# Kernel optimization log

Hardware: AMD Instinct MI355X
Metric: run time of the kernel (lower is better)

The kernel has to match this reference:

```python
import jax, jax.numpy as jnp
import numpy as np

B, NUM_ANCHORS, NUM_CLASSES = 32, 15130, 81
SCALE_XY, SCALE_WH = 0.1, 0.2
CRITERIA, MAX_OUT, SCORE_THRESH = 0.5, 200, 0.05


def setup_inputs() -> dict:
    key = jax.random.key(0)
    k1, k2, k3, k4 = jax.random.split(key, 4)
    ploc = jax.random.normal(k1, (B, 4, NUM_ANCHORS), dtype=jnp.float32)
    plabel = jax.random.normal(k2, (B, NUM_CLASSES, NUM_ANCHORS), dtype=jnp.float32)
    # default boxes in (cx, cy, w, h) form, all in [0, 1]
    xy = jax.random.uniform(k3, (NUM_ANCHORS, 2), dtype=jnp.float32, minval=0.05, maxval=0.95)
    wh = jax.random.uniform(k4, (NUM_ANCHORS, 2), dtype=jnp.float32, minval=0.02, maxval=0.3)
    dboxes_xywh = jnp.concatenate([xy, wh], axis=-1)
    return {"ploc": ploc, "plabel": plabel, "dboxes_xywh": dboxes_xywh}


def _iou(a, b):
    # a: [M,4] ltrb, b: [K,4] ltrb -> [M,K]
    lt = jnp.maximum(a[:, None, :2], b[None, :, :2])
    rb = jnp.minimum(a[:, None, 2:], b[None, :, 2:])
    wh = jnp.clip(rb - lt, 0.0)
    inter = wh[..., 0] * wh[..., 1]
    area_a = (a[:, 2] - a[:, 0]) * (a[:, 3] - a[:, 1])
    area_b = (b[:, 2] - b[:, 0]) * (b[:, 3] - b[:, 1])
    return inter / (area_a[:, None] + area_b[None, :] - inter + 1e-12)


def _decode(ploc, plabel, dboxes_xywh):
    # scale_back_batch: ploc [B,4,N] -> ltrb boxes [B,N,4]
    b = jnp.transpose(ploc, (0, 2, 1))
    xy = b[..., :2] * SCALE_XY * dboxes_xywh[:, 2:] + dboxes_xywh[:, :2]
    wh = jnp.exp(b[..., 2:] * SCALE_WH) * dboxes_xywh[:, 2:]
    ltrb = jnp.concatenate([xy - 0.5 * wh, xy + 0.5 * wh], axis=-1)  # [B,N,4]
    probs = jnp.transpose(jax.nn.softmax(plabel, axis=1), (0, 2, 1))  # [B,N,C]
    return ltrb, probs


def _nms_per_class(scores_c, boxes):
    # scores_c: [N], boxes: [N,4]
    s = jnp.where(scores_c > SCORE_THRESH, scores_c, 0.0)
    vals, idx = jax.lax.top_k(s, MAX_OUT)  # descending, matches score-sorted greedy order
    bx = boxes[idx]  # [MAX_OUT,4]
    iou = _iou(bx, bx)  # [MAX_OUT,MAX_OUT]
    later = jnp.arange(MAX_OUT)

    def body(i, keep):
        active = keep[i] & (vals[i] > 0.0)
        suppress = active & (iou[i] >= CRITERIA) & (later > i)
        return keep & ~suppress

    keep = jax.lax.fori_loop(0, MAX_OUT, body, jnp.ones((MAX_OUT,), bool))
    keep = keep & (vals > 0.0)
    return jnp.where(keep, vals, 0.0), bx


def _decode_single(probs_i, boxes_i):
    # skip background class 0
    cls_scores = probs_i[:, 1:].T  # [C-1, N]
    vals, bx = jax.vmap(_nms_per_class, in_axes=(0, None))(cls_scores, boxes_i)
    c1 = NUM_CLASSES - 1
    flat_v = vals.reshape(-1)                 # [(C-1)*MAX_OUT]
    flat_b = bx.reshape(-1, 4)
    labels = jnp.repeat(jnp.arange(1, c1 + 1, dtype=jnp.int32), MAX_OUT)
    top_v, top_i = jax.lax.top_k(flat_v, MAX_OUT)
    return flat_b[top_i], labels[top_i], top_v


def reference(ploc, plabel, dboxes_xywh):
    ltrb, probs = _decode(ploc, plabel, dboxes_xywh)
    boxes_out, labels_out, scores_out = jax.vmap(_decode_single)(probs, ltrb)
    return boxes_out, labels_out, scores_out
```

## Files before the change

kernel.cpp:

```cpp
#include <hip/hip_runtime.h>
#include <math.h>

namespace {
constexpr int BATCH = 32;
constexpr int NANCH = 15130;
constexpr int NCLS  = 81;
constexpr int C1    = 80;
constexpr int MAXO  = 200;
constexpr int APB   = 256;
constexpr int NBLKA = (NANCH + APB - 1) / APB;
constexpr int CAPK2 = 512;
constexpr int CAP   = 1024;
constexpr int CAPB  = 768;
constexpr int NWORD = 4;
constexpr int NBIN  = 2048;
constexpr int NBINK2 = 768;
constexpr unsigned BINBASE = 0x3D000000u;
constexpr int IMGCAP = C1 * MAXO;
}

#define SCORE_TH 0.05f
#define IOU_TH   0.5f

typedef unsigned long long u64;

__device__ __forceinline__ u64 shflx64(u64 v, int mask) {
    int lo = __shfl_xor((int)(unsigned)(v & 0xffffffffull), mask, 64);
    int hi = __shfl_xor((int)(unsigned)(v >> 32), mask, 64);
    return ((u64)(unsigned)hi << 32) | (unsigned)lo;
}

__device__ __forceinline__ void bitonic_desc(u64* keys, int P,
                                             int tid, int nthr) {
    for (int k = 2; k <= P; k <<= 1) {
        for (int j = k >> 1; j > 0; j >>= 1) {
            for (int i = tid; i < P; i += nthr) {
                int ixj = i ^ j;
                if (ixj > i) {
                    u64 a = keys[i], c = keys[ixj];
                    bool up = ((i & k) == 0);
                    if (up ? (a < c) : (a > c)) { keys[i] = c; keys[ixj] = a; }
                }
            }
            __syncthreads();
        }
    }
}

__device__ __forceinline__ u64 regsort256(u64 key, u64* lds, int tid) {
    for (int k = 2; k <= 256; k <<= 1) {
        for (int j = k >> 1; j > 0; j >>= 1) {
            u64 pv;
            if (j < 64) {
                pv = shflx64(key, j);
            } else {
                lds[tid] = key;
                __syncthreads();
                pv = lds[tid ^ j];
            }
            bool up = ((tid & k) == 0);
            bool lt = ((tid & j) == 0);
            u64 mx = (key > pv) ? key : pv;
            u64 mn = (key > pv) ? pv : key;
            key = (up == lt) ? mx : mn;
            if (j >= 64) __syncthreads();
        }
    }
    return key;
}

__global__ __launch_bounds__(256, 3) void ssd_decode_stats(
    const float* __restrict__ ploc, const float* __restrict__ plabel,
    const float* __restrict__ dboxes,
    float* __restrict__ ltrb, float* __restrict__ rowmax,
    float* __restrict__ rowsum,
    int* __restrict__ cntg, u64* __restrict__ bucket) {
#pragma clang fp contract(off)
    __shared__ int lcnt[C1], lbase[C1], lrank[C1];

    const int tid = threadIdx.x;
    const int b   = blockIdx.x / NBLKA;
    const int n0  = (blockIdx.x % NBLKA) * APB;
    const int n   = n0 + tid;
    const bool act = (n < NANCH);

    if (tid < C1) lcnt[tid] = 0;

    float x[NCLS];
    if (act) {
        const float* pl = ploc + (size_t)b * 4 * NANCH + n;
        float px = pl[0], py = pl[NANCH], pw = pl[2 * NANCH],
              ph = pl[3 * NANCH];
        float4 db = reinterpret_cast<const float4*>(dboxes)[n];
        float cx = px * 0.1f * db.z + db.x;
        float cy = py * 0.1f * db.w + db.y;
        float w  = expf(pw * 0.2f) * db.z;
        float h  = expf(ph * 0.2f) * db.w;
        float4 o;
        o.x = cx - 0.5f * w; o.y = cy - 0.5f * h;
        o.z = cx + 0.5f * w; o.w = cy + 0.5f * h;
        reinterpret_cast<float4*>(ltrb)[(size_t)b * NANCH + n] = o;

        const float* pb = plabel + (size_t)b * NCLS * NANCH + n;
#pragma unroll
        for (int c = 0; c < NCLS; ++c) x[c] = pb[(size_t)c * NANCH];

        float m = -INFINITY;
#pragma unroll
        for (int c = 0; c < NCLS; ++c) m = fmaxf(m, x[c]);
#pragma unroll
        for (int c = 0; c < NCLS; ++c) x[c] = expf(x[c] - m);
        float s = 0.f;
#pragma unroll
        for (int c = 0; c < NCLS; ++c) s += x[c];
        rowmax[(size_t)b * NANCH + n] = m;
        rowsum[(size_t)b * NANCH + n] = s;

#pragma unroll
        for (int c = 1; c < NCLS; ++c) {
            x[c] = x[c] / s;
            if (x[c] > SCORE_TH) atomicAdd(&lcnt[c - 1], 1);
        }
    }
    __syncthreads();

    if (tid < C1) {
        int cn = lcnt[tid];
        lbase[tid] = (cn > 0) ? atomicAdd(&cntg[b * C1 + tid], cn) : 0;
        lrank[tid] = 0;
    }
    __syncthreads();

    if (act) {
#pragma unroll
        for (int c = 1; c < NCLS; ++c) {
            if (x[c] > SCORE_TH) {
                int r = atomicAdd(&lrank[c - 1], 1);
                int pos = lbase[c - 1] + r;
                if (pos < CAPB)
                    bucket[(size_t)(b * C1 + (c - 1)) * CAPB + pos] =
                        ((u64)__float_as_uint(x[c]) << 32)
                        | (u64)(0xFFFFFFFFu - (unsigned)n);
            }
        }
    }
}

__global__ __launch_bounds__(256, 8) void ssd_class_nms(
    const float* __restrict__ plabel, const float* __restrict__ rowmax,
    const float* __restrict__ rowsum, const float* __restrict__ ltrb,
    const int* __restrict__ cntg, const u64* __restrict__ bucket,
    float* __restrict__ pcVals, float* __restrict__ pcBoxes,
    int* __restrict__ imgcnt, u64* __restrict__ imglist) {
    __shared__ u64 cand[CAPK2];
    __shared__ unsigned int hist[NBINK2];
    __shared__ float4 box4[MAXO];
    __shared__ float areas[MAXO], vs[MAXO];
    __shared__ u64 supflat[MAXO * NWORD];
    __shared__ u64 keepw[NWORD], vmaskS[NWORD];
    __shared__ int wtot[4];
    __shared__ int cnt, fillcnt, cutbin, kcnt, kbase;

    const int tid  = threadIdx.x;
    const int lane = tid & 63;
    const int wv   = tid >> 6;
    const int b    = blockIdx.x / C1;
    const int cls  = blockIdx.x % C1 + 1;
    const int bc   = b * C1 + (cls - 1);

    for (int i = tid; i < NBINK2; i += 256) hist[i] = 0u;
    if (tid == 0) { cnt = 0; fillcnt = 0; cutbin = 1; kcnt = 0; }
    __syncthreads();

    const float* pl = plabel + ((size_t)b * NCLS + cls) * NANCH;
    const float* rm = rowmax + (size_t)b * NANCH;
    const float* rs = rowsum + (size_t)b * NANCH;
    const u64* bkt = bucket + (size_t)bc * CAPB;

    const int gcount = cntg[bc];
    const bool ovf = (gcount > CAPB);
    int gathered;

    if (!ovf) {
        const int count = gcount;
        for (int i = tid; i < count; i += 256) {
            unsigned bits = (unsigned)(bkt[i] >> 32);
            unsigned bin = ((bits - BINBASE) >> 16) + 1u;
            if (bin > NBINK2 - 1) bin = NBINK2 - 1;
            atomicAdd(&hist[bin], 1u);
        }
        __syncthreads();

        const int base = tid * 3;
        int loc = (int)hist[base] + (int)hist[base + 1] + (int)hist[base + 2];
        int sfx = loc;
        for (int off = 1; off < 64; off <<= 1) {
            int t = __shfl_down(sfx, off, 64);
            if (lane + off < 64) sfx += t;
        }
        if (lane == 0) wtot[wv] = sfx;
        __syncthreads();
        int crossSuf = 0;
        for (int w2 = wv + 1; w2 < 4; ++w2) crossSuf += wtot[w2];
        const int nztot = wtot[0] + wtot[1] + wtot[2] + wtot[3];
        {
            int S = (sfx - loc) + crossSuf;
            for (int k = 2; k >= 0; --k) {
                int binv = (int)hist[base + k];
                int Sk = S + binv;
                int bin = base + k;
                if (bin >= 1 && Sk >= MAXO && S < MAXO) cutbin = bin;
                S = Sk;
            }
        }
        __syncthreads();
        const int B = (nztot >= MAXO) ? cutbin : 1;

        for (int i = tid; i < count; i += 256) {
            u64 k = bkt[i];
            unsigned bits = (unsigned)(k >> 32);
            unsigned bin = ((bits - BINBASE) >> 16) + 1u;
            if (bin > NBINK2 - 1) bin = NBINK2 - 1;
            if ((int)bin >= B) {
                int pos = atomicAdd(&cnt, 1);
                if (pos < CAPK2) cand[pos] = k;
            }
        }
        __syncthreads();
        gathered = min(cnt, CAPK2);
    } else {
        for (int n = tid; n < NANCH; n += 256) {
            float p = expf(pl[n] - rm[n]) / rs[n];
            if (p > SCORE_TH) {
                int pos = atomicAdd(&cnt, 1);
                if (pos < CAPK2)
                    cand[pos] = ((u64)__float_as_uint(p) << 32)
                              | (u64)(0xFFFFFFFFu - (unsigned)n);
            }
        }
        __syncthreads();
        gathered = min(cnt, CAPK2);
    }

    u64 key;
    if (gathered <= 256) {
        key = (tid < gathered) ? cand[tid] : 0ull;
        key = regsort256(key, cand, tid);
    } else {
        for (int i = gathered + tid; i < CAPK2; i += 256) cand[i] = 0ull;
        __syncthreads();
        bitonic_desc(cand, CAPK2, tid, 256);
        key = cand[tid];
    }

    if (gathered < MAXO) {
        int* scanb = (int*)hist;
        cand[tid] = key;
        __syncthreads();
        const int need = MAXO - gathered;
        for (int base2 = 0; base2 < NANCH; base2 += 256) {
            if (fillcnt >= need) break;
            int n = base2 + tid;
            int flag = 0;
            if (n < NANCH) {
                float p = expf(pl[n] - rm[n]) / rs[n];
                flag = (p <= SCORE_TH) ? 1 : 0;
            }
            scanb[tid] = flag;
            __syncthreads();
            for (int off = 1; off < 256; off <<= 1) {
                int v  = scanb[tid];
                int vp = (tid >= off) ? scanb[tid - off] : 0;
                __syncthreads();
                scanb[tid] = v + vp;
                __syncthreads();
            }
            int excl = scanb[tid] - flag;
            if (flag && (fillcnt + excl) < need)
                cand[gathered + fillcnt + excl] =
                    (u64)(0xFFFFFFFFu - (unsigned)n);
            __syncthreads();
            if (tid == 0) fillcnt += scanb[255];
            __syncthreads();
        }
        __syncthreads();
        key = cand[tid];
    }

    if (tid < MAXO) {
#pragma clang fp contract(off)
        float sc   = __uint_as_float((unsigned)(key >> 32));
        unsigned n = 0xFFFFFFFFu - (unsigned)(key & 0xFFFFFFFFull);
        float4 bb =
            reinterpret_cast<const float4*>(ltrb)[(size_t)b * NANCH + n];
        box4[tid] = bb;
        areas[tid] = (bb.z - bb.x) * (bb.w - bb.y);
        vs[tid] = sc;
    }
    {
        bool pred = (tid < MAXO) ?
            (__uint_as_float((unsigned)(key >> 32)) > 0.f) : false;
        u64 bal = __ballot(pred);
        if (lane == 0) vmaskS[wv] = bal;
    }
    __syncthreads();

    if (tid < MAXO) {
#pragma clang fp contract(off)
        const int i = tid;
        float4 bi = box4[i];
        float ai = areas[i];
        for (int w = 0; w < NWORD; ++w) {
            int j0 = max(i + 1, w * 64);
            int j1 = min(MAXO, w * 64 + 64);
            u64 m = 0ull;
            for (int j = j0; j < j1; ++j) {
                float4 bj = box4[j];
                float l = fmaxf(bi.x, bj.x);
                float t = fmaxf(bi.y, bj.y);
                float r = fminf(bi.z, bj.z);
                float d = fminf(bi.w, bj.w);
                float ww = fmaxf(r - l, 0.f);
                float hh = fmaxf(d - t, 0.f);
                float inter = ww * hh;
                float denom = ai + areas[j] - inter + 1e-12f;
                float t2 = inter + inter;
                bool sup_t = (t2 >= denom);
                bool band = (t2 < denom) && (t2 > denom * 0.99999952f);
                if (__any(band))
                    sup_t = band ? ((inter / denom) >= IOU_TH) : sup_t;
                m |= sup_t ? (1ull << (j - w * 64)) : 0ull;
            }
            supflat[i * NWORD + w] = m;
        }
    }
    __syncthreads();

    if (tid == 0) {
        u64 v0 = vmaskS[0], v1 = vmaskS[1], v2 = vmaskS[2], v3 = vmaskS[3];
        u64 k0 = ~0ull, k1 = ~0ull, k2 = ~0ull, k3 = ~0ull;
        for (int w = 0; w < 4; ++w) {
            u64 vw = (w == 0) ? v0 : (w == 1) ? v1 : (w == 2) ? v2 : v3;
            u64 kw = (w == 0) ? k0 : (w == 1) ? k1 : (w == 2) ? k2 : k3;
            u64 cur = kw & vw;
            while (cur) {
                int bit = __builtin_ctzll(cur);
                int i = w * 64 + bit;
                k0 &= ~supflat[i * NWORD + 0];
                k1 &= ~supflat[i * NWORD + 1];
                k2 &= ~supflat[i * NWORD + 2];
                k3 &= ~supflat[i * NWORD + 3];
                kw = (w == 0) ? k0 : (w == 1) ? k1 : (w == 2) ? k2 : k3;
                u64 above = (bit == 63) ? 0ull : (~0ull << (bit + 1));
                cur = kw & vw & above;
            }
        }
        keepw[0] = k0; keepw[1] = k1; keepw[2] = k2; keepw[3] = k3;
    }
    __syncthreads();

    bool kp = false;
    if (tid < MAXO) {
        kp = (keepw[tid >> 6] >> (tid & 63)) & 1ull;
        pcVals[(size_t)bc * MAXO + tid] = (kp && vs[tid] > 0.f) ? vs[tid] : 0.f;
        reinterpret_cast<float4*>(pcBoxes + (size_t)bc * MAXO * 4)[tid] =
            box4[tid];
    }

    bool keep_me = (tid < MAXO) && kp && (vs[tid] > 0.f);
    int r = -1;
    if (keep_me) r = atomicAdd(&kcnt, 1);
    __syncthreads();
    if (tid == 0) kbase = (kcnt > 0) ? atomicAdd(&imgcnt[b], kcnt) : 0;
    __syncthreads();
    if (keep_me) {
        unsigned g = (unsigned)((cls - 1) * MAXO + tid);
        imglist[(size_t)b * IMGCAP + kbase + r] =
            ((u64)__float_as_uint(vs[tid]) << 32) | (u64)(0xFFFFFFFFu - g);
    }
}

__global__ __launch_bounds__(256) void ssd_final_topk(
    const float* __restrict__ pcVals, const float* __restrict__ pcBoxes,
    const int* __restrict__ imgcnt, const u64* __restrict__ imglist,
    float* __restrict__ out) {
    __shared__ unsigned int hist[NBIN];
    __shared__ u64 cand[CAP];
    __shared__ int wtot[4];
    __shared__ int cnt, cutbin, nztot;

    const int tid  = threadIdx.x;
    const int lane = tid & 63;
    const int wv   = tid >> 6;
    const int b    = blockIdx.x;
    const int TOT  = C1 * MAXO;
    const float* pv = pcVals + (size_t)b * TOT;
    const int NZ   = imgcnt[b];

    for (int i = tid; i < NBIN; i += 256) hist[i] = 0u;
    if (tid == 0) { cnt = 0; cutbin = 1; }
    __syncthreads();

    int count;
    if (NZ >= MAXO) {
        const u64* lst = imglist + (size_t)b * IMGCAP;
        for (int i = tid; i < NZ; i += 256) {
            unsigned bits = (unsigned)(lst[i] >> 32);
            unsigned bin = ((bits - BINBASE) >> 15) + 1u;
            if (bin > NBIN - 1) bin = NBIN - 1;
            atomicAdd(&hist[bin], 1u);
        }
        __syncthreads();

        const int base = tid * 8;
        int loc = 0;
        for (int k = 0; k < 8; ++k) loc += (int)hist[base + k];
        int sfx = loc;
        for (int off = 1; off < 64; off <<= 1) {
            int t = __shfl_down(sfx, off, 64);
            if (lane + off < 64) sfx += t;
        }
        if (lane == 0) wtot[wv] = sfx;
        __syncthreads();
        int crossSuf = 0;
        for (int w2 = wv + 1; w2 < 4; ++w2) crossSuf += wtot[w2];
        {
            int S = (sfx - loc) + crossSuf;
            for (int k = 7; k >= 0; --k) {
                int binv = (int)hist[base + k];
                int Sk = S + binv;
                int bin = base + k;
                if (bin >= 1 && Sk >= MAXO && S < MAXO) cutbin = bin;
                S = Sk;
            }
        }
        __syncthreads();
        const int B = cutbin;

        for (int i = tid; i < NZ; i += 256) {
            u64 k = lst[i];
            unsigned bits = (unsigned)(k >> 32);
            unsigned bin = ((bits - BINBASE) >> 15) + 1u;
            if (bin > NBIN - 1) bin = NBIN - 1;
            if ((int)bin >= B) {
                int pos = atomicAdd(&cnt, 1);
                if (pos < CAP) cand[pos] = k;
            }
        }
        __syncthreads();
        count = min(cnt, CAP);
    } else {
        for (int g = tid; g < TOT; g += 256) {
            float v = pv[g];
            if (v > 0.f) {
                unsigned bits = __float_as_uint(v);
                unsigned bin = ((bits - BINBASE) >> 15) + 1u;
                if (bin > NBIN - 1) bin = NBIN - 1;
                atomicAdd(&hist[bin], 1u);
            }
        }
        __syncthreads();
        const int base = tid * 8;
        int loc = 0;
        for (int k = 0; k < 8; ++k) loc += (int)hist[base + k];
        int sfx = loc;
        for (int off = 1; off < 64; off <<= 1) {
            int t = __shfl_down(sfx, off, 64);
            if (lane + off < 64) sfx += t;
        }
        if (lane == 0) wtot[wv] = sfx;
        __syncthreads();
        int crossSuf = 0;
        for (int w2 = wv + 1; w2 < 4; ++w2) crossSuf += wtot[w2];
        if (tid == 0) nztot = wtot[0] + wtot[1] + wtot[2] + wtot[3];
        {
            int S = (sfx - loc) + crossSuf;
            for (int k = 7; k >= 0; --k) {
                int binv = (int)hist[base + k];
                int Sk = S + binv;
                int bin = base + k;
                if (bin >= 1 && Sk >= MAXO && S < MAXO) cutbin = bin;
                S = Sk;
            }
        }
        __syncthreads();
        int B = (nztot >= MAXO) ? cutbin : 1;

        for (int g = tid; g < TOT; g += 256) {
            float v = pv[g];
            if (v > 0.f) {
                unsigned bits = __float_as_uint(v);
                unsigned bin = ((bits - BINBASE) >> 15) + 1u;
                if (bin > NBIN - 1) bin = NBIN - 1;
                if ((int)bin >= B) {
                    int pos = atomicAdd(&cnt, 1);
                    if (pos < CAP)
                        cand[pos] = ((u64)bits << 32)
                                  | (u64)(0xFFFFFFFFu - (unsigned)g);
                }
            }
        }
        __syncthreads();
        count = min(cnt, CAP);

        if (count < MAXO) {
            if (tid == 0) {
                int c = count;
                for (int g = 0; g < TOT && c < MAXO; ++g) {
                    if (!(pv[g] > 0.f)) {
                        cand[c++] = (u64)(0xFFFFFFFFu - (unsigned)g);
                    }
                }
                cnt = c;
            }
            __syncthreads();
            count = min(cnt, CAP);
        }
    }

    u64 key;
    if (count <= 256) {
        key = (tid < count) ? cand[tid] : 0ull;
        key = regsort256(key, cand, tid);
    } else {
        int P = 256; while (P < count) P <<= 1;
        for (int i = count + tid; i < P; i += 256) cand[i] = 0ull;
        __syncthreads();
        bitonic_desc(cand, P, tid, 256);
        key = cand[tid];
    }

    if (tid < MAXO) {
        float sc      = __uint_as_float((unsigned)(key >> 32));
        unsigned flat = 0xFFFFFFFFu - (unsigned)(key & 0xFFFFFFFFull);
        int cls = (int)(flat / MAXO) + 1;
        const float4 bb =
            reinterpret_cast<const float4*>(pcBoxes)[(size_t)b * TOT + flat];
        reinterpret_cast<float4*>(out)[(size_t)b * MAXO + tid] = bb;
        out[(size_t)BATCH * MAXO * 4 + (size_t)b * MAXO + tid] = (float)cls;
        out[(size_t)BATCH * MAXO * 5 + (size_t)b * MAXO + tid] = sc;
    }
}

extern "C" void kernel_launch(void* const* d_in, const int* in_sizes, int n_in,
                              void* d_out, int out_size, void* d_ws,
                              size_t ws_size, hipStream_t stream) {
    const float* ploc   = (const float*)d_in[0];
    const float* plabel = (const float*)d_in[1];
    const float* dboxes = (const float*)d_in[2];
    float* out = (float*)d_out;

    float* ws      = (float*)d_ws;
    float* ltrb    = ws;
    float* rowmax  = ltrb   + (size_t)BATCH * NANCH * 4;
    float* rowsum  = rowmax + (size_t)BATCH * NANCH;
    float* pcVals  = rowsum + (size_t)BATCH * NANCH;
    float* pcBoxes = pcVals + (size_t)BATCH * C1 * MAXO;
    int*   cntg    = (int*)(pcBoxes + (size_t)BATCH * C1 * MAXO * 4);
    int*   imgcnt  = cntg + BATCH * C1;
    char*  after   = (char*)(imgcnt + BATCH);
    u64* bucket = (u64*)(after + ((16 - (((size_t)after) & 15)) & 15));
    u64* imglist = bucket + (size_t)BATCH * C1 * CAPB;

    hipMemsetAsync(cntg, 0, (size_t)(BATCH * C1 + BATCH) * sizeof(int), stream);
    ssd_decode_stats<<<BATCH * NBLKA, APB, 0, stream>>>(
        ploc, plabel, dboxes, ltrb, rowmax, rowsum, cntg, bucket);
    ssd_class_nms<<<BATCH * C1, 256, 0, stream>>>(
        plabel, rowmax, rowsum, ltrb, cntg, bucket, pcVals, pcBoxes,
        imgcnt, imglist);
    ssd_final_topk<<<BATCH, 256, 0, stream>>>(
        pcVals, pcBoxes, imgcnt, imglist, out);
}
```

Baseline: 238.6 us.

## Parallelize IoU suppression mask build across lanes using ballots per row

Rebuilds the pairwise IoU suppression bitmask so that each lane handles one column j and each wave iterates over rows i, producing each 64-bit word with a wave ballot. Before, one thread per row walked a serial j loop. Only the triangular region is computed, and the greedy scan skips reading words it can never need. This spreads the O(MAXO^2) IoU work across all four wavefronts and removes divergent per-thread loops. In exchange it adds ballot overhead and a serial i loop per wave.

```diff
diff --git a/kernel.cpp b/kernel.cpp
--- a/kernel.cpp
+++ b/kernel.cpp
@@ -305,17 +305,18 @@
     }
     __syncthreads();
 
-    if (tid < MAXO) {
+    {
 #pragma clang fp contract(off)
-        const int i = tid;
-        float4 bi = box4[i];
-        float ai = areas[i];
-        for (int w = 0; w < NWORD; ++w) {
-            int j0 = max(i + 1, w * 64);
-            int j1 = min(MAXO, w * 64 + 64);
-            u64 m = 0ull;
-            for (int j = j0; j < j1; ++j) {
-                float4 bj = box4[j];
+#pragma unroll
+        for (int c = 0; c < NWORD; ++c) {
+            const int jc = c * 64 + lane;
+            const bool jv = (jc < MAXO);
+            const float4 bj = box4[jv ? jc : 0];
+            const float aj = areas[jv ? jc : 0];
+            const int iend = (MAXO < c * 64 + 64) ? MAXO : (c * 64 + 64);
+            for (int i = wv; i < iend; i += 4) {
+                float4 bi = box4[i];
+                float ai = areas[i];
                 float l = fmaxf(bi.x, bj.x);
                 float t = fmaxf(bi.y, bj.y);
                 float r = fminf(bi.z, bj.z);
@@ -323,15 +324,24 @@
                 float ww = fmaxf(r - l, 0.f);
                 float hh = fmaxf(d - t, 0.f);
                 float inter = ww * hh;
-                float denom = ai + areas[j] - inter + 1e-12f;
+                float denom = ai + aj - inter + 1e-12f;
                 float t2 = inter + inter;
-                bool sup_t = (t2 >= denom);
-                bool band = (t2 < denom) && (t2 > denom * 0.99999952f);
-                if (__any(band))
-                    sup_t = band ? ((inter / denom) >= IOU_TH) : sup_t;
-                m |= sup_t ? (1ull << (j - w * 64)) : 0ull;
-            }
-            supflat[i * NWORD + w] = m;
+                u64 supb  = __ballot(t2 >= denom);
+                u64 bandb = __ballot((t2 < denom) &&
+                                     (t2 > denom * 0.99999952f));
+                u64 valid = (c == 3) ? ((1ull << (MAXO - 192)) - 1ull) : ~0ull;
+                if (i >= c * 64) {
+                    int sh = i - c * 64 + 1;
+                    valid &= (sh >= 64) ? 0ull : (~0ull << sh);
+                }
+                supb &= valid;
+                bandb &= valid & ~supb;
+                if (bandb) {
+                    u64 divb = __ballot(jv && ((inter / denom) >= IOU_TH));
+                    supb = (supb & ~bandb) | (divb & bandb);
+                }
+                if (lane == 0) supflat[i * NWORD + c] = supb;
+            }
         }
     }
     __syncthreads();
@@ -346,9 +356,9 @@
             while (cur) {
                 int bit = __builtin_ctzll(cur);
                 int i = w * 64 + bit;
-                k0 &= ~supflat[i * NWORD + 0];
-                k1 &= ~supflat[i * NWORD + 1];
-                k2 &= ~supflat[i * NWORD + 2];
+                if (w == 0) k0 &= ~supflat[i * NWORD + 0];
+                if (w <= 1) k1 &= ~supflat[i * NWORD + 1];
+                if (w <= 2) k2 &= ~supflat[i * NWORD + 2];
                 k3 &= ~supflat[i * NWORD + 3];
                 kw = (w == 0) ? k0 : (w == 1) ? k1 : (w == 2) ? k2 : k3;
                 u64 above = (bit == 63) ? 0ull : (~0ull << (bit + 1));
```

New measurement: 241.2 us. Within noise of the previous version (+1.1%).

## Replace full IoU bitmask NMS with iterative keep-driven suppression rounds

Applied to the files above, without the earlier changes.

Drops the precomputed 200x200 suppression bitmask and the serial single-thread scan. NMS now runs greedily: each round picks the next kept candidate, every thread tests its own box against it, and a ballot clears suppressed bits. This does IoU work only for kept boxes and frees shared memory, which may raise occupancy. The cost is two block barriers per kept box, which can be many when few boxes overlap, and an exact division per test.

```diff
diff --git a/kernel.cpp b/kernel.cpp
--- a/kernel.cpp
+++ b/kernel.cpp
@@ -156,10 +156,9 @@
     __shared__ unsigned int hist[NBINK2];
     __shared__ float4 box4[MAXO];
     __shared__ float areas[MAXO], vs[MAXO];
-    __shared__ u64 supflat[MAXO * NWORD];
-    __shared__ u64 keepw[NWORD], vmaskS[NWORD];
+    __shared__ u64 keepw[NWORD], vmaskS[NWORD], supRow[NWORD];
     __shared__ int wtot[4];
-    __shared__ int cnt, fillcnt, cutbin, kcnt, kbase;
+    __shared__ int cnt, fillcnt, cutbin, kcnt, kbase, curI;
 
     const int tid  = threadIdx.x;
     const int lane = tid & 63;
@@ -287,87 +286,96 @@
         key = cand[tid];
     }
 
+    float4 bjr = make_float4(0.f, 0.f, 0.f, 0.f);
+    float ajr = 0.f, vsr = 0.f;
     if (tid < MAXO) {
 #pragma clang fp contract(off)
-        float sc   = __uint_as_float((unsigned)(key >> 32));
+        vsr = __uint_as_float((unsigned)(key >> 32));
         unsigned n = 0xFFFFFFFFu - (unsigned)(key & 0xFFFFFFFFull);
-        float4 bb =
-            reinterpret_cast<const float4*>(ltrb)[(size_t)b * NANCH + n];
-        box4[tid] = bb;
-        areas[tid] = (bb.z - bb.x) * (bb.w - bb.y);
-        vs[tid] = sc;
+        bjr = reinterpret_cast<const float4*>(ltrb)[(size_t)b * NANCH + n];
+        ajr = (bjr.z - bjr.x) * (bjr.w - bjr.y);
+        box4[tid] = bjr;
+        areas[tid] = ajr;
+        vs[tid] = vsr;
     }
     {
-        bool pred = (tid < MAXO) ?
-            (__uint_as_float((unsigned)(key >> 32)) > 0.f) : false;
+        bool pred = (tid < MAXO) && (vsr > 0.f);
         u64 bal = __ballot(pred);
         if (lane == 0) vmaskS[wv] = bal;
     }
-    __syncthreads();
-
-    if (tid < MAXO) {
+    if (tid == 0) {
+        keepw[0] = ~0ull; keepw[1] = ~0ull; keepw[2] = ~0ull; keepw[3] = ~0ull;
+    }
+    __syncthreads();
+
+    if (tid == 0) {
+        int ni = -1;
+        u64 c0 = keepw[0] & vmaskS[0];
+        if (c0) ni = __builtin_ctzll(c0);
+        else {
+            u64 c1 = keepw[1] & vmaskS[1];
+            if (c1) ni = 64 + __builtin_ctzll(c1);
+            else {
+                u64 c2 = keepw[2] & vmaskS[2];
+                if (c2) ni = 128 + __builtin_ctzll(c2);
+                else {
+                    u64 c3 = keepw[3] & vmaskS[3];
+                    if (c3) ni = 192 + __builtin_ctzll(c3);
+                }
+            }
+        }
+        curI = ni;
+    }
+    __syncthreads();
+
+    while (true) {
+        const int i = curI;
+        if (i < 0) break;
+        bool sup = false;
+        if (tid > i && tid < MAXO) {
 #pragma clang fp contract(off)
-        const int i = tid;
-        float4 bi = box4[i];
-        float ai = areas[i];
-        for (int w = 0; w < NWORD; ++w) {
-            int j0 = max(i + 1, w * 64);
-            int j1 = min(MAXO, w * 64 + 64);
-            u64 m = 0ull;
-            for (int j = j0; j < j1; ++j) {
-                float4 bj = box4[j];
-                float l = fmaxf(bi.x, bj.x);
-                float t = fmaxf(bi.y, bj.y);
-                float r = fminf(bi.z, bj.z);
-                float d = fminf(bi.w, bj.w);
-                float ww = fmaxf(r - l, 0.f);
-                float hh = fmaxf(d - t, 0.f);
-                float inter = ww * hh;
-                float denom = ai + areas[j] - inter + 1e-12f;
-                float t2 = inter + inter;
-                bool sup_t = (t2 >= denom);
-                bool band = (t2 < denom) && (t2 > denom * 0.99999952f);
-                if (__any(band))
-                    sup_t = band ? ((inter / denom) >= IOU_TH) : sup_t;
-                m |= sup_t ? (1ull << (j - w * 64)) : 0ull;
-            }
-            supflat[i * NWORD + w] = m;
-        }
-    }
-    __syncthreads();
-
-    if (tid == 0) {
-        u64 v0 = vmaskS[0], v1 = vmaskS[1], v2 = vmaskS[2], v3 = vmaskS[3];
-        u64 k0 = ~0ull, k1 = ~0ull, k2 = ~0ull, k3 = ~0ull;
-        for (int w = 0; w < 4; ++w) {
-            u64 vw = (w == 0) ? v0 : (w == 1) ? v1 : (w == 2) ? v2 : v3;
-            u64 kw = (w == 0) ? k0 : (w == 1) ? k1 : (w == 2) ? k2 : k3;
-            u64 cur = kw & vw;
-            while (cur) {
-                int bit = __builtin_ctzll(cur);
-                int i = w * 64 + bit;
-                k0 &= ~supflat[i * NWORD + 0];
-                k1 &= ~supflat[i * NWORD + 1];
-                k2 &= ~supflat[i * NWORD + 2];
-                k3 &= ~supflat[i * NWORD + 3];
-                kw = (w == 0) ? k0 : (w == 1) ? k1 : (w == 2) ? k2 : k3;
-                u64 above = (bit == 63) ? 0ull : (~0ull << (bit + 1));
-                cur = kw & vw & above;
-            }
-        }
-        keepw[0] = k0; keepw[1] = k1; keepw[2] = k2; keepw[3] = k3;
-    }
-    __syncthreads();
+            float4 bi = box4[i];
+            float ai = areas[i];
+            float l = fmaxf(bi.x, bjr.x);
+            float t = fmaxf(bi.y, bjr.y);
+            float r = fminf(bi.z, bjr.z);
+            float d = fminf(bi.w, bjr.w);
+            float ww = fmaxf(r - l, 0.f);
+            float hh = fmaxf(d - t, 0.f);
+            float inter = ww * hh;
+            float denom = ai + ajr - inter + 1e-12f;
+            sup = ((inter / denom) >= IOU_TH);
+        }
+        u64 bal = __ballot(sup);
+        if (lane == 0) supRow[wv] = bal;
+        __syncthreads();
+        if (tid == 0) {
+            keepw[0] &= ~supRow[0];
+            keepw[1] &= ~supRow[1];
+            keepw[2] &= ~supRow[2];
+            keepw[3] &= ~supRow[3];
+            int w = i >> 6, bit = i & 63;
+            u64 above = (bit == 63) ? 0ull : (~0ull << (bit + 1));
+            int ni = -1;
+            u64 cur = keepw[w] & vmaskS[w] & above;
+            while (true) {
+                if (cur) { ni = w * 64 + __builtin_ctzll(cur); break; }
+                if (++w >= 4) break;
+                cur = keepw[w] & vmaskS[w];
+            }
+            curI = ni;
+        }
+        __syncthreads();
+    }
 
     bool kp = false;
     if (tid < MAXO) {
         kp = (keepw[tid >> 6] >> (tid & 63)) & 1ull;
-        pcVals[(size_t)bc * MAXO + tid] = (kp && vs[tid] > 0.f) ? vs[tid] : 0.f;
-        reinterpret_cast<float4*>(pcBoxes + (size_t)bc * MAXO * 4)[tid] =
-            box4[tid];
-    }
-
-    bool keep_me = (tid < MAXO) && kp && (vs[tid] > 0.f);
+        pcVals[(size_t)bc * MAXO + tid] = (kp && vsr > 0.f) ? vsr : 0.f;
+        reinterpret_cast<float4*>(pcBoxes + (size_t)bc * MAXO * 4)[tid] = bjr;
+    }
+
+    bool keep_me = (tid < MAXO) && kp && (vsr > 0.f);
     int r = -1;
     if (keep_me) r = atomicAdd(&kcnt, 1);
     __syncthreads();
@@ -376,7 +384,7 @@
     if (keep_me) {
         unsigned g = (unsigned)((cls - 1) * MAXO + tid);
         imglist[(size_t)b * IMGCAP + kbase + r] =
-            ((u64)__float_as_uint(vs[tid]) << 32) | (u64)(0xFFFFFFFFu - g);
+            ((u64)__float_as_uint(vsr) << 32) | (u64)(0xFFFFFFFFu - g);
     }
 }
 
```

Measured after the change: 303.5 us. 1.27x slower.
